# Performance work log

Measured on AMD Instinct MI355X. Metric: run time of the kernel, lower is better.

## Reference

```python
import jax, jax.numpy as jnp
import numpy as np

SHIFT, REDUCE = 0, 1
B, T, E, H, V, O = 128, 256, 300, 256, 32000, 5


def _rand_trans(rng, n_tok):
    # valid shift-reduce sequence: n_tok SHIFTs, n_tok-1 REDUCEs
    seq = np.empty(2 * n_tok - 1, np.int32)
    shifts = 0
    depth = 0
    for i in range(2 * n_tok - 1):
        if shifts < n_tok and (depth < 2 or rng.random() < 0.6):
            seq[i] = SHIFT; shifts += 1; depth += 1
        else:
            seq[i] = REDUCE; depth -= 1
    return seq


def setup_inputs() -> dict:
    key = jax.random.key(0)
    ks = jax.random.split(key, 10)
    rng = np.random.default_rng(0)
    x_ids = jax.random.randint(ks[0], (B, T), 0, V)
    transitions = jnp.asarray(np.stack([_rand_trans(rng, T) for _ in range(B)], axis=1))  # [2T-1, B]
    u = lambda k, shape, s: jax.random.uniform(k, shape, jnp.float32, -s, s)
    sE = 1.0 / np.sqrt(E)
    sH = 1.0 / np.sqrt(H)
    embed_table = (jax.random.normal(ks[1], (V, E), jnp.float32) * 0.1).at[1].set(0.0)  # padding_idx=1
    return dict(
        x_ids=x_ids, transitions=transitions, embed_table=embed_table,
        Wp=u(ks[2], (H, E), sE), bp=u(ks[3], (H,), sE),
        Wg=u(ks[4], (H, E), sE), bg=u(ks[5], (H,), sE),
        Wr=u(ks[6], (5 * H, 2 * H), sH), br=u(ks[7], (5 * H,), sH),
        Wo=u(ks[8], (O, H), sH), bo=u(ks[9], (O,), sH),
    )


def reference(x_ids, transitions, embed_table, Wp, bp, Wg, bg, Wr, br, Wo, bo):
    Hh = Wp.shape[0]
    Bn, Tn = x_ids.shape
    emb = embed_table[x_ids]                                   # [B,T,E]
    c_buf = jnp.einsum('bte,he->bth', emb, Wp) + bp            # proj_x
    h_buf = jnp.tanh(c_buf) * jax.nn.sigmoid(jnp.einsum('bte,he->bth', emb, Wg) + bg)
    buffers = jnp.concatenate([h_buf, c_buf], axis=-1)         # [B,T,2H]
    bidx = jnp.arange(Bn)

    def cell(left, right):
        hl, cl = jnp.split(left, 2, axis=-1)
        hr, cr = jnp.split(right, 2, axis=-1)
        proj = jnp.concatenate([hl, hr], axis=-1) @ Wr.T + br  # [B,5H]
        i, fl, fr, g, o = jnp.split(proj, 5, axis=-1)
        c_new = jax.nn.sigmoid(i) * jnp.tanh(g) + jax.nn.sigmoid(fl) * cl + jax.nn.sigmoid(fr) * cr
        h_new = jax.nn.sigmoid(o) * jnp.tanh(c_new)
        return jnp.concatenate([h_new, c_new], axis=-1)

    def step(carry, t_batch):
        stack, sptr, bptr = carry
        is_shift = (t_batch == SHIFT)
        shifted = buffers[bidx, bptr - 1]                      # buffer.pop() = last token first
        left = stack[bidx, sptr - 2]
        right = stack[bidx, sptr - 1]
        reduced = cell(left, right)
        new_state = jnp.where(is_shift[:, None], shifted, reduced)
        new_sptr = jnp.where(is_shift, sptr + 1, sptr - 1)
        new_bptr = jnp.where(is_shift, bptr - 1, bptr)
        stack = stack.at[bidx, new_sptr - 1].set(new_state)    # push (shift or reduce result)
        return (stack, new_sptr, new_bptr), None

    init = (jnp.zeros((Bn, Tn, 2 * Hh), buffers.dtype),
            jnp.zeros((Bn,), jnp.int32), jnp.full((Bn,), Tn, jnp.int32))
    (stack, sptr, _), _ = jax.lax.scan(step, init, transitions)
    final_h = stack[bidx, sptr - 1][:, :Hh]                    # root h
    logits = final_h @ Wo.T + bo                               # dropout is identity in eval
    return logits
```

## Files before the change

### kernel.cpp

```cpp
#include <hip/hip_runtime.h>
#include <hip/hip_bf16.h>

#define B 128
#define T 256
#define E 300
#define HH 256
#define O 5
#define NSTEP (2*T - 1)
#define NINT 255
#define NG 8
#define PSTR 41
#define IOFF 16777216u
#define LMAX_DIRECT 176
#define CHUNK 96
#define BAR_STRIDE 16
#define BAR_WORDS ((32 + 2) * BAR_STRIDE)

__device__ __forceinline__ float sigm(float x) { return 1.f / (1.f + __expf(-x)); }

__device__ __forceinline__ void grid_barrier(unsigned* bar, int myN) {
  __syncthreads();
  if (threadIdx.x == 0) {
    __threadfence();
    const int per_sub = (int)(gridDim.x >> 5);
    const int s = (int)(blockIdx.x & 31);
    unsigned r = atomicAdd(&bar[s * BAR_STRIDE], 1u);
    if (r == (unsigned)(myN * per_sub - 1)) {
      unsigned q = atomicAdd(&bar[32 * BAR_STRIDE], 1u);
      if (q == (unsigned)(myN * 32 - 1)) {
        atomicAdd(&bar[33 * BAR_STRIDE], 1u);
      }
    }
    while (__hip_atomic_load(&bar[33 * BAR_STRIDE], __ATOMIC_ACQUIRE,
                             __HIP_MEMORY_SCOPE_AGENT) < (unsigned)myN) {
      __builtin_amdgcn_s_sleep(2);
    }
    __threadfence();
  }
  __syncthreads();
}

__global__ __launch_bounds__(256) void k_transpose(
    const float* __restrict__ Wp, const float* __restrict__ Wg,
    const float* __restrict__ Wr, float* __restrict__ WcT,
    float* __restrict__ W4) {
  int idx = blockIdx.x * 256 + threadIdx.x;
  if (idx < HH * E) {
    int h = idx / E;
    int e = idx % E;
    WcT[e * 512 + h]       = Wp[idx];
    WcT[e * 512 + 256 + h] = Wg[idx];
  }
  if (idx < 5 * HH * 2 * HH) {
    int j = idx / 512;
    int k = idx % 512;
    W4[((size_t)(k >> 2) * 1280 + j) * 4 + (k & 3)] = Wr[idx];
  }
}

#define TT 16
__global__ __launch_bounds__(256) void k_buffers(
    const int* __restrict__ x_ids, const float* __restrict__ embed,
    const float* __restrict__ WcT, const float* __restrict__ bp,
    const float* __restrict__ bg, float* __restrict__ buffers) {
  __shared__ __align__(16) float lds[TT * E];
  const int b  = blockIdx.y;
  const int t0 = blockIdx.x * TT;
  const int tid = threadIdx.x;

  for (int i = tid; i < TT * E; i += 256) {
    int t = i / E;
    int e = i % E;
    int id = x_ids[b * T + t0 + t];
    lds[i] = embed[(size_t)id * E + e];
  }
  __syncthreads();

  const int h = tid;
  float accP[TT], accG[TT];
#pragma unroll
  for (int t = 0; t < TT; ++t) { accP[t] = bp[h]; accG[t] = bg[h]; }

  const float4* lds4 = (const float4*)lds;
  for (int e4 = 0; e4 < E / 4; ++e4) {
    const float* wc = WcT + (e4 * 4) * 512 + h;
    float wp0 = wc[0],    wg0 = wc[256];
    float wp1 = wc[512],  wg1 = wc[768];
    float wp2 = wc[1024], wg2 = wc[1280];
    float wp3 = wc[1536], wg3 = wc[1792];
#pragma unroll
    for (int t = 0; t < TT; ++t) {
      float4 x = lds4[t * (E / 4) + e4];
      accP[t] = fmaf(x.x, wp0, accP[t]); accG[t] = fmaf(x.x, wg0, accG[t]);
      accP[t] = fmaf(x.y, wp1, accP[t]); accG[t] = fmaf(x.y, wg1, accG[t]);
      accP[t] = fmaf(x.z, wp2, accP[t]); accG[t] = fmaf(x.z, wg2, accG[t]);
      accP[t] = fmaf(x.w, wp3, accP[t]); accG[t] = fmaf(x.w, wg3, accG[t]);
    }
  }

#pragma unroll
  for (int t = 0; t < TT; ++t) {
    float c  = accP[t];
    float hb = tanhf(c) * sigm(accG[t]);
    size_t base = ((size_t)b * T + t0 + t) * 512;
    buffers[base + h]       = hb;
    buffers[base + 256 + h] = c;
  }
}

__global__ __launch_bounds__(128) void k_prep(
    const int* __restrict__ trans, int* __restrict__ meta,
    int* __restrict__ levCnt, int* __restrict__ levOff, int* __restrict__ maxLevG,
    int* __restrict__ rootA, unsigned* __restrict__ worklist,
    unsigned* __restrict__ bar) {
  extern __shared__ char dynls[];
  unsigned short* stkL = (unsigned short*)dynls;
  unsigned char*  levL = (unsigned char*)(dynls + 65536);
  int*            tch  = (int*)(dynls + 65536 + 32640);
  __shared__ int cnt[256];
  __shared__ int off[256];
  __shared__ int cur[256];
  const int b = threadIdx.x;
  for (int i = b; i < 256; i += 128) cnt[i] = 0;
  for (int i = b; i < BAR_WORDS; i += 128) bar[i] = 0u;
  __syncthreads();

  int sp = 0, bp = T, r = 0;
  for (int c0 = 0; c0 < NSTEP; c0 += CHUNK) {
    const int cend = min(NSTEP - c0, CHUNK);
    __syncthreads();
    for (int i = b; i < cend * 128; i += 128) tch[i] = trans[c0 * 128 + i];
    __syncthreads();
    for (int s = 0; s < cend; ++s) {
      int tr = tch[s * 128 + b];
      if (tr == 0) {
        stkL[sp * 128 + b] = (unsigned short)(bp - 1);
        sp++; bp--;
      } else {
        int idR = stkL[(sp - 1) * 128 + b];
        int idL = stkL[(sp - 2) * 128 + b];
        sp -= 2;
        int lL = (idL < 256) ? 0 : (int)levL[(idL - 256) * 128 + b];
        int lR = (idR < 256) ? 0 : (int)levL[(idR - 256) * 128 + b];
        int lev = max(lL, lR) + 1;
        levL[r * 128 + b] = (unsigned char)lev;
        meta[b * NINT + r] = idL | (idR << 9) | (lev << 18);
        atomicAdd(&cnt[lev], 1);
        stkL[sp * 128 + b] = (unsigned short)(256 + r);
        sp++; r++;
      }
    }
  }
  rootA[b] = (int)stkL[0 * 128 + b];
  __syncthreads();

  if (b == 0) {
    int acc = 0, ml = 1;
    for (int l = 0; l < 256; ++l) {
      off[l] = acc; acc += cnt[l];
      if (cnt[l] > 0) ml = l;
    }
    *maxLevG = ml;
  }
  __syncthreads();
  for (int i = b; i < 256; i += 128) { levCnt[i] = cnt[i]; levOff[i] = off[i]; cur[i] = off[i]; }
  __syncthreads();

  for (int i = 0; i < NINT; ++i) {
    int lev = (int)levL[i * 128 + b];
    int pos = atomicAdd(&cur[lev], 1);
    worklist[pos] = (unsigned)((b << 9) | (256 + i));
  }
}

__device__ __forceinline__ void do_level(
    int cnt, int woff,
    const float* __restrict__ W4, const float* __restrict__ br,
    const int* __restrict__ meta, const unsigned* __restrict__ worklist,
    float* __restrict__ states, float* smem) {
  const int tid  = threadIdx.x;
  const int hcol = tid & 63;
  const int kq   = tid >> 6;

  const int ngrp = (cnt + NG - 1) / NG;
  const int items = ngrp << 2;

  for (int item = blockIdx.x; item < items; item += gridDim.x) {
    const int grp = item >> 2;
    const int h0  = (item & 3) << 6;
    __syncthreads();

    unsigned offL[NG], offR[NG], offD[NG];
#pragma unroll
    for (int n = 0; n < NG; ++n) {
      int wi = woff + grp * NG + n;
      if (wi >= woff + cnt) wi = woff + cnt - 1;
      unsigned w = worklist[wi];
      int node = __builtin_amdgcn_readfirstlane((int)(w & 511u));
      int bb   = __builtin_amdgcn_readfirstlane((int)(w >> 9));
      int m    = __builtin_amdgcn_readfirstlane(meta[bb * NINT + node - 256]);
      int il = m & 511, ir = (m >> 9) & 511;
      offL[n] = (il < 256) ? ((unsigned)(bb * T + il) << 9)
                           : (IOFF + ((unsigned)(bb * NINT + il - 256) << 9));
      offR[n] = (ir < 256) ? ((unsigned)(bb * T + ir) << 9)
                           : (IOFF + ((unsigned)(bb * NINT + ir - 256) << 9));
      offD[n] = IOFF + ((unsigned)(bb * NINT + node - 256) << 9);
    }

    float* xs = smem;
#pragma unroll
    for (int n = 0; n < NG; ++n) {
      xs[n * 512 + tid]       = states[(size_t)offL[n] + tid];
      xs[n * 512 + 256 + tid] = states[(size_t)offR[n] + tid];
    }
    __syncthreads();

    float a0[NG], a1[NG], a2[NG], a3[NG], a4[NG];
#pragma unroll
    for (int n = 0; n < NG; ++n) { a0[n]=0.f; a1[n]=0.f; a2[n]=0.f; a3[n]=0.f; a4[n]=0.f; }

    const float4* W4v = (const float4*)W4;
    const int jb = h0 + hcol;
    const int k4end = (kq << 5) + 32;
    for (int k4 = kq << 5; k4 < k4end; ++k4) {
      const size_t kb4 = (size_t)k4 * 1280 + jb;
      float4 w0 = W4v[kb4];
      float4 w1 = W4v[kb4 + 256];
      float4 w2 = W4v[kb4 + 512];
      float4 w3 = W4v[kb4 + 768];
      float4 w4 = W4v[kb4 + 1024];
#pragma unroll
      for (int n = 0; n < NG; ++n) {
        float4 xv = *(const float4*)&xs[n * 512 + (k4 << 2)];
        float s0 = a0[n], s1 = a1[n], s2 = a2[n], s3 = a3[n], s4 = a4[n];
        s0 = fmaf(w0.x, xv.x, s0); s0 = fmaf(w0.y, xv.y, s0);
        s0 = fmaf(w0.z, xv.z, s0); s0 = fmaf(w0.w, xv.w, s0);
        s1 = fmaf(w1.x, xv.x, s1); s1 = fmaf(w1.y, xv.y, s1);
        s1 = fmaf(w1.z, xv.z, s1); s1 = fmaf(w1.w, xv.w, s1);
        s2 = fmaf(w2.x, xv.x, s2); s2 = fmaf(w2.y, xv.y, s2);
        s2 = fmaf(w2.z, xv.z, s2); s2 = fmaf(w2.w, xv.w, s2);
        s3 = fmaf(w3.x, xv.x, s3); s3 = fmaf(w3.y, xv.y, s3);
        s3 = fmaf(w3.z, xv.z, s3); s3 = fmaf(w3.w, xv.w, s3);
        s4 = fmaf(w4.x, xv.x, s4); s4 = fmaf(w4.y, xv.y, s4);
        s4 = fmaf(w4.z, xv.z, s4); s4 = fmaf(w4.w, xv.w, s4);
        a0[n] = s0; a1[n] = s1; a2[n] = s2; a3[n] = s3; a4[n] = s4;
      }
    }
    __syncthreads();

    if (kq >= 1) {
      float* pp = smem + (kq - 1) * (64 * PSTR) + hcol * PSTR;
#pragma unroll
      for (int n = 0; n < NG; ++n) {
        pp[n]          = a0[n];
        pp[NG + n]     = a1[n];
        pp[2 * NG + n] = a2[n];
        pp[3 * NG + n] = a3[n];
        pp[4 * NG + n] = a4[n];
      }
    }
    __syncthreads();

    if (kq == 0) {
      const int habs = h0 + hcol;
      const float b0 = br[habs];
      const float b1 = br[256 + habs];
      const float b2 = br[512 + habs];
      const float b3 = br[768 + habs];
      const float b4 = br[1024 + habs];
#pragma unroll
      for (int n = 0; n < NG; ++n) {
        const float* q0 = smem + 0 * (64 * PSTR) + hcol * PSTR;
        const float* q1 = smem + 1 * (64 * PSTR) + hcol * PSTR;
        const float* q2 = smem + 2 * (64 * PSTR) + hcol * PSTR;
        float p0 = a0[n] + q0[n]          + q1[n]          + q2[n]          + b0;
        float p1 = a1[n] + q0[NG + n]     + q1[NG + n]     + q2[NG + n]     + b1;
        float p2 = a2[n] + q0[2 * NG + n] + q1[2 * NG + n] + q2[2 * NG + n] + b2;
        float p3 = a3[n] + q0[3 * NG + n] + q1[3 * NG + n] + q2[3 * NG + n] + b3;
        float p4 = a4[n] + q0[4 * NG + n] + q1[4 * NG + n] + q2[4 * NG + n] + b4;
        float cl = states[(size_t)offL[n] + 256 + habs];
        float cr = states[(size_t)offR[n] + 256 + habs];
        float ci  = sigm(p0);
        float cfl = sigm(p1);
        float cfr = sigm(p2);
        float tg  = tanhf(p3);
        float co  = sigm(p4);
        float cn  = ci * tg + cfl * cl + cfr * cr;
        float hn  = co * tanhf(cn);
        states[(size_t)offD[n] + habs]       = hn;
        states[(size_t)offD[n] + 256 + habs] = cn;
      }
    }
  }
}

__global__ __launch_bounds__(256, 4) void k_level(
    int lev, const float* __restrict__ W4, const float* __restrict__ br,
    const int* __restrict__ meta, const int* __restrict__ levCnt,
    const int* __restrict__ levOff, const int* __restrict__ maxLevG,
    const unsigned* __restrict__ worklist, float* __restrict__ states) {
  __shared__ float smem[3 * 64 * PSTR];
  if (lev > *maxLevG) return;
  const int cnt = levCnt[lev];
  if (cnt == 0) return;
  do_level(cnt, levOff[lev], W4, br, meta, worklist, states, smem);
}

__global__ __launch_bounds__(256, 2) void k_catchall(
    const float* __restrict__ W4, const float* __restrict__ br,
    const int* __restrict__ meta, const int* __restrict__ levCnt,
    const int* __restrict__ levOff, const int* __restrict__ maxLevG,
    const unsigned* __restrict__ worklist, float* __restrict__ states,
    unsigned* __restrict__ bar) {
  __shared__ float smem[3 * 64 * PSTR];
  const int maxLev = *maxLevG;
  if (maxLev <= LMAX_DIRECT) return;
  for (int lev = LMAX_DIRECT + 1; lev <= maxLev; ++lev) {
    do_level(levCnt[lev], levOff[lev], W4, br, meta, worklist, states, smem);
    grid_barrier(bar, lev - LMAX_DIRECT);
  }
}

__global__ __launch_bounds__(256) void k_out(
    const float* __restrict__ Wo, const float* __restrict__ bo,
    const int* __restrict__ rootA, const float* __restrict__ states,
    float* __restrict__ out) {
  const int b = blockIdx.x;
  const int tid = threadIdx.x;
  __shared__ float red[256];
  int rid = rootA[b];
  unsigned hoff = (rid < 256) ? ((unsigned)(b * T + rid) << 9)
                              : (IOFF + ((unsigned)(b * NINT + rid - 256) << 9));
  float hj = states[(size_t)hoff + tid];
  for (int m = 0; m < O; ++m) {
    red[tid] = Wo[m * HH + tid] * hj;
    __syncthreads();
    for (int off = 128; off > 0; off >>= 1) {
      if (tid < off) red[tid] += red[tid + off];
      __syncthreads();
    }
    if (tid == 0) out[b * O + m] = red[0] + bo[m];
    __syncthreads();
  }
}

extern "C" void kernel_launch(void* const* d_in, const int* in_sizes, int n_in,
                              void* d_out, int out_size, void* d_ws, size_t ws_size,
                              hipStream_t stream) {
  const int*   x_ids = (const int*)d_in[0];
  const int*   trans = (const int*)d_in[1];
  const float* embed = (const float*)d_in[2];
  const float* Wp    = (const float*)d_in[3];
  const float* bp    = (const float*)d_in[4];
  const float* Wg    = (const float*)d_in[5];
  const float* bg    = (const float*)d_in[6];
  const float* Wr    = (const float*)d_in[7];
  const float* br    = (const float*)d_in[8];
  const float* Wo    = (const float*)d_in[9];
  const float* bo    = (const float*)d_in[10];
  float* out = (float*)d_out;

  float* ws       = (float*)d_ws;
  float* WcT      = ws;
  float* W4       = WcT + 300 * 512;
  float* states   = W4 + 512 * 1280;
  int*   meta     = (int*)(states + (size_t)IOFF + (size_t)B * NINT * 512);
  int*   levCnt   = meta + B * NINT;
  int*   levOff   = levCnt + 256;
  int*   maxLevG  = levOff + 256;
  int*   rootA    = maxLevG + 1;
  unsigned* worklist = (unsigned*)(rootA + B);
  unsigned* bar   = worklist + B * NINT;

  k_transpose<<<(5 * HH * 2 * HH + 255) / 256, 256, 0, stream>>>(Wp, Wg, Wr, WcT, W4);
  k_buffers<<<dim3(T / TT, B), 256, 0, stream>>>(x_ids, embed, WcT, bp, bg, states);

  const size_t prep_lds = 65536 + 32640 + (size_t)CHUNK * 128 * 4;
  k_prep<<<1, 128, prep_lds, stream>>>(trans, meta, levCnt, levOff, maxLevG, rootA,
                                       worklist, bar);

  for (int lev = 1; lev <= LMAX_DIRECT; ++lev) {
    int g = (lev <= 16) ? 512 : (lev <= 48) ? 256 : 128;
    k_level<<<g, 256, 0, stream>>>(lev, W4, br, meta, levCnt, levOff, maxLevG,
                                   worklist, states);
  }

  {
    void* args[] = {(void*)&W4, (void*)&br, (void*)&meta, (void*)&levCnt, (void*)&levOff,
                    (void*)&maxLevG, (void*)&worklist, (void*)&states, (void*)&bar};
    hipLaunchCooperativeKernel((void*)k_catchall, dim3(512), dim3(256), args, 0, stream);
  }

  k_out<<<B, 256, 0, stream>>>(Wo, bo, rootA, states, out);
}
```

Baseline: 3.512 ms.

## Give each thread a full output column instead of splitting K across warps

```diff
diff --git a/kernel.cpp b/kernel.cpp
--- a/kernel.cpp
+++ b/kernel.cpp
@@ -9,7 +9,6 @@
 #define NSTEP (2*T - 1)
 #define NINT 255
 #define NG 8
-#define PSTR 41
 #define IOFF 16777216u
 #define LMAX_DIRECT 176
 #define CHUNK 96
@@ -177,17 +176,11 @@
     int cnt, int woff,
     const float* __restrict__ W4, const float* __restrict__ br,
     const int* __restrict__ meta, const unsigned* __restrict__ worklist,
-    float* __restrict__ states, float* smem) {
-  const int tid  = threadIdx.x;
-  const int hcol = tid & 63;
-  const int kq   = tid >> 6;
-
+    float* __restrict__ states, float* xs) {
+  const int tid = threadIdx.x;
   const int ngrp = (cnt + NG - 1) / NG;
-  const int items = ngrp << 2;
-
-  for (int item = blockIdx.x; item < items; item += gridDim.x) {
-    const int grp = item >> 2;
-    const int h0  = (item & 3) << 6;
+
+  for (int grp = blockIdx.x; grp < ngrp; grp += gridDim.x) {
     __syncthreads();
 
     unsigned offL[NG], offR[NG], offD[NG];
@@ -207,7 +200,6 @@
       offD[n] = IOFF + ((unsigned)(bb * NINT + node - 256) << 9);
     }
 
-    float* xs = smem;
 #pragma unroll
     for (int n = 0; n < NG; ++n) {
       xs[n * 512 + tid]       = states[(size_t)offL[n] + tid];
@@ -220,10 +212,9 @@
     for (int n = 0; n < NG; ++n) { a0[n]=0.f; a1[n]=0.f; a2[n]=0.f; a3[n]=0.f; a4[n]=0.f; }
 
     const float4* W4v = (const float4*)W4;
-    const int jb = h0 + hcol;
-    const int k4end = (kq << 5) + 32;
-    for (int k4 = kq << 5; k4 < k4end; ++k4) {
-      const size_t kb4 = (size_t)k4 * 1280 + jb;
+    const float4* xs4 = (const float4*)xs;
+    for (int k4 = 0; k4 < 128; ++k4) {
+      const size_t kb4 = (size_t)k4 * 1280 + tid;
       float4 w0 = W4v[kb4];
       float4 w1 = W4v[kb4 + 256];
       float4 w2 = W4v[kb4 + 512];
@@ -231,7 +222,7 @@
       float4 w4 = W4v[kb4 + 1024];
 #pragma unroll
       for (int n = 0; n < NG; ++n) {
-        float4 xv = *(const float4*)&xs[n * 512 + (k4 << 2)];
+        float4 xv = xs4[n * 128 + k4];
         float s0 = a0[n], s1 = a1[n], s2 = a2[n], s3 = a3[n], s4 = a4[n];
         s0 = fmaf(w0.x, xv.x, s0); s0 = fmaf(w0.y, xv.y, s0);
         s0 = fmaf(w0.z, xv.z, s0); s0 = fmaf(w0.w, xv.w, s0);
@@ -246,50 +237,25 @@
         a0[n] = s0; a1[n] = s1; a2[n] = s2; a3[n] = s3; a4[n] = s4;
       }
     }
-    __syncthreads();
-
-    if (kq >= 1) {
-      float* pp = smem + (kq - 1) * (64 * PSTR) + hcol * PSTR;
-#pragma unroll
-      for (int n = 0; n < NG; ++n) {
-        pp[n]          = a0[n];
-        pp[NG + n]     = a1[n];
-        pp[2 * NG + n] = a2[n];
-        pp[3 * NG + n] = a3[n];
-        pp[4 * NG + n] = a4[n];
-      }
-    }
-    __syncthreads();
-
-    if (kq == 0) {
-      const int habs = h0 + hcol;
-      const float b0 = br[habs];
-      const float b1 = br[256 + habs];
-      const float b2 = br[512 + habs];
-      const float b3 = br[768 + habs];
-      const float b4 = br[1024 + habs];
-#pragma unroll
-      for (int n = 0; n < NG; ++n) {
-        const float* q0 = smem + 0 * (64 * PSTR) + hcol * PSTR;
-        const float* q1 = smem + 1 * (64 * PSTR) + hcol * PSTR;
-        const float* q2 = smem + 2 * (64 * PSTR) + hcol * PSTR;
-        float p0 = a0[n] + q0[n]          + q1[n]          + q2[n]          + b0;
-        float p1 = a1[n] + q0[NG + n]     + q1[NG + n]     + q2[NG + n]     + b1;
-        float p2 = a2[n] + q0[2 * NG + n] + q1[2 * NG + n] + q2[2 * NG + n] + b2;
-        float p3 = a3[n] + q0[3 * NG + n] + q1[3 * NG + n] + q2[3 * NG + n] + b3;
-        float p4 = a4[n] + q0[4 * NG + n] + q1[4 * NG + n] + q2[4 * NG + n] + b4;
-        float cl = states[(size_t)offL[n] + 256 + habs];
-        float cr = states[(size_t)offR[n] + 256 + habs];
-        float ci  = sigm(p0);
-        float cfl = sigm(p1);
-        float cfr = sigm(p2);
-        float tg  = tanhf(p3);
-        float co  = sigm(p4);
-        float cn  = ci * tg + cfl * cl + cfr * cr;
-        float hn  = co * tanhf(cn);
-        states[(size_t)offD[n] + habs]       = hn;
-        states[(size_t)offD[n] + 256 + habs] = cn;
-      }
+
+    const float b0 = br[tid];
+    const float b1 = br[256 + tid];
+    const float b2 = br[512 + tid];
+    const float b3 = br[768 + tid];
+    const float b4 = br[1024 + tid];
+#pragma unroll
+    for (int n = 0; n < NG; ++n) {
+      float cl = states[(size_t)offL[n] + 256 + tid];
+      float cr = states[(size_t)offR[n] + 256 + tid];
+      float ci  = sigm(a0[n] + b0);
+      float cfl = sigm(a1[n] + b1);
+      float cfr = sigm(a2[n] + b2);
+      float tg  = tanhf(a3[n] + b3);
+      float co  = sigm(a4[n] + b4);
+      float cn  = ci * tg + cfl * cl + cfr * cr;
+      float hn  = co * tanhf(cn);
+      states[(size_t)offD[n] + tid]       = hn;
+      states[(size_t)offD[n] + 256 + tid] = cn;
     }
   }
 }
@@ -299,11 +265,11 @@
     const int* __restrict__ meta, const int* __restrict__ levCnt,
     const int* __restrict__ levOff, const int* __restrict__ maxLevG,
     const unsigned* __restrict__ worklist, float* __restrict__ states) {
-  __shared__ float smem[3 * 64 * PSTR];
+  __shared__ __align__(16) float xs[NG * 512];
   if (lev > *maxLevG) return;
   const int cnt = levCnt[lev];
   if (cnt == 0) return;
-  do_level(cnt, levOff[lev], W4, br, meta, worklist, states, smem);
+  do_level(cnt, levOff[lev], W4, br, meta, worklist, states, xs);
 }
 
 __global__ __launch_bounds__(256, 2) void k_catchall(
@@ -312,11 +278,11 @@
     const int* __restrict__ levOff, const int* __restrict__ maxLevG,
     const unsigned* __restrict__ worklist, float* __restrict__ states,
     unsigned* __restrict__ bar) {
-  __shared__ float smem[3 * 64 * PSTR];
+  __shared__ __align__(16) float xs[NG * 512];
   const int maxLev = *maxLevG;
   if (maxLev <= LMAX_DIRECT) return;
   for (int lev = LMAX_DIRECT + 1; lev <= maxLev; ++lev) {
-    do_level(levCnt[lev], levOff[lev], W4, br, meta, worklist, states, smem);
+    do_level(levCnt[lev], levOff[lev], W4, br, meta, worklist, states, xs);
     grid_barrier(bar, lev - LMAX_DIRECT);
   }
 }
@@ -380,7 +346,7 @@
                                        worklist, bar);
 
   for (int lev = 1; lev <= LMAX_DIRECT; ++lev) {
-    int g = (lev <= 16) ? 512 : (lev <= 48) ? 256 : 128;
+    int g = (lev <= 4) ? 1024 : (lev <= 16) ? 512 : (lev <= 48) ? 128 : 64;
     k_level<<<g, 256, 0, stream>>>(lev, W4, br, meta, levCnt, levOff, maxLevG,
                                    worklist, states);
   }
```

After: 9.929 ms. 183% more time.
